# Kernel optimization log

Hardware: AMD Instinct MI355X
Metric: run time of the kernel (lower is better)

Reference implementation:

```python
import jax, jax.numpy as jnp
import numpy as np

T, IO, H, M = 8192, 32, 256, 4  # timesteps, io_width, hidden_width, max ponder steps
EPS = 0.01  # ACT halting epsilon


def setup_inputs() -> dict:
    key = jax.random.key(0)
    ks = jax.random.split(key, 8)
    sc = 0.05
    return {
        "x": jax.random.normal(ks[0], (T, IO), jnp.float32),
        "h0": jnp.zeros((H,), jnp.float32),                       # act1_h initial state
        "Wp": jax.random.normal(ks[1], (H, IO), jnp.float32) * sc,  # input_processing Linear
        "bp": jnp.zeros((H,), jnp.float32),
        "Wx": jax.random.normal(ks[2], (H, H + 1), jnp.float32) * sc,  # ACT cell input weights (+1 first-step flag)
        "Ws": jax.random.normal(ks[3], (H, H), jnp.float32) * sc,      # ACT cell recurrent weights
        "b": jnp.zeros((H,), jnp.float32),
        "wh": jax.random.normal(ks[4], (H,), jnp.float32) * sc,        # halting unit
        "bh": jnp.float32(1.0),
        "Wo": jax.random.normal(ks[5], (IO, H), jnp.float32) * sc,     # ACT output projection
        "bo": jnp.zeros((IO,), jnp.float32),
    }


def reference(x, h0, Wp, bp, Wx, Ws, b, wh, bh, Wo, bo):
    # Faithful translation: per-timestep loop (lax.scan) over the sequence; each step
    # runs input_processing then an ACT (Graves) ponder loop with max M=4 steps.
    # io_noise is identity in eval mode. attention_beam_width=1 => line == current point.
    T_ = x.shape[0]

    def step(carry, x_t):
        h, pc = carry
        lin1 = Wp @ x_t + bp  # [H]
        s = h
        cum = jnp.float32(0.0)
        acc_s = jnp.zeros_like(h)
        acc_y = jnp.zeros_like(bo)
        n_up = jnp.float32(0.0)
        rem = jnp.float32(0.0)
        still = jnp.bool_(True)
        for n in range(M):  # fixed small ponder loop, masked ACT halting
            flag = jnp.full((1,), 1.0 if n == 0 else 0.0, lin1.dtype)
            inp = jnp.concatenate([lin1, flag])  # [H+1]
            s = jnp.tanh(Wx @ inp + Ws @ s + b)
            p = jax.nn.sigmoid(wh @ s + bh)
            halt = (cum + p > 1.0 - EPS) | (n == M - 1)
            w = jnp.where(still, jnp.where(halt, 1.0 - cum, p), 0.0)
            acc_s = acc_s + w * s
            acc_y = acc_y + w * (Wo @ s + bo)
            rem = rem + jnp.where(still & halt, 1.0 - cum, 0.0)
            n_up = n_up + jnp.where(still, 1.0, 0.0)
            cum = cum + w
            still = still & jnp.logical_not(halt)
        ponder = n_up + rem  # N(t) + R(t)
        pc = (pc + ponder) / jnp.float32(T_)  # matches the in-loop division in the original forward
        return (acc_s, pc), acc_y

    (_, pc), ys = jax.lax.scan(step, (h0, jnp.float32(0.0)), x)
    return ys, pc
```

## Files before the change

### kernel.cpp

```cpp
#include <hip/hip_runtime.h>


#define T_  8192
#define IO_ 32
#define H_  256

typedef __attribute__((ext_vector_type(2))) float v2f;

template<int CTRL>
__device__ __forceinline__ float dpp_addf(float x) {
    int xi = __builtin_bit_cast(int, x);
    int d = __builtin_amdgcn_update_dpp(xi, xi, CTRL, 0xF, 0xF, false);
    return x + __builtin_bit_cast(float, d);
}
template<int CTRL>
__device__ __forceinline__ float dpp_get(float x) {
    int xi = __builtin_bit_cast(int, x);
    int d = __builtin_amdgcn_update_dpp(xi, xi, CTRL, 0xF, 0xF, false);
    return __builtin_bit_cast(float, d);
}
__device__ __forceinline__ float swz_xor4(float x) {
    return __builtin_bit_cast(float,
        __builtin_amdgcn_ds_swizzle(__builtin_bit_cast(int, x), 0x101F));
}
__device__ __forceinline__ void bar_lds() {
    asm volatile("s_waitcnt lgkmcnt(0)\n\ts_barrier" ::: "memory");
    __builtin_amdgcn_sched_barrier(0);
}

__device__ __forceinline__ float mv_reduce(const v2f (&wt)[8][8], const v2f (&sc)[8]) {
    float v[8];
    #pragma unroll
    for (int k = 0; k < 8; ++k) {
        v2f a = wt[k][0] * sc[0];
        #pragma unroll
        for (int q = 1; q < 8; ++q) a += wt[k][q] * sc[q];
        v[k] = a.x + a.y;
    }
    v[0] += dpp_get<0x128>(v[4]);
    v[1] += dpp_get<0x128>(v[5]);
    v[2] += dpp_get<0x128>(v[6]);
    v[3] += dpp_get<0x128>(v[7]);
    v[0] += dpp_get<0x4E>(v[2]);
    v[1] += dpp_get<0x4E>(v[3]);
    v[0] += swz_xor4(v[1]);
    v[0] += dpp_get<0xB1>(v[0]);
    return v[0];
}

__global__ void k_prep(const float* __restrict__ Wx,
                       const float* __restrict__ Wp,
                       const float* __restrict__ bp,
                       const float* __restrict__ b,
                       float* __restrict__ WxpT, float* __restrict__ cvec) {
    int h = blockIdx.x;
    int t = threadIdx.x;
    __shared__ float wxrow[H_];
    for (int j = t; j < H_; j += 64) wxrow[j] = Wx[h * (H_ + 1) + j];
    __syncthreads();
    if (t < IO_) {
        float acc = 0.0f;
        for (int j = 0; j < H_; ++j) acc += wxrow[j] * Wp[j * IO_ + t];
        WxpT[t * H_ + h] = acc;
    } else if (t == IO_) {
        float acc = b[h];
        for (int j = 0; j < H_; ++j) acc += wxrow[j] * bp[j];
        cvec[h] = acc;
    }
}

__global__ void k_u(const float* __restrict__ x,
                    const float* __restrict__ WxpT,
                    const float* __restrict__ cvec,
                    float* __restrict__ U) {
    int t0 = blockIdx.x * 8;
    int tid = threadIdx.x;
    __shared__ float xsf[8 * IO_];
    xsf[tid] = x[(size_t)t0 * IO_ + tid];
    __syncthreads();
    int h = tid;
    float base = cvec[h];
    const float L2E2 = 2.8853900817779268f;
    for (int tt = 0; tt < 8; ++tt) {
        float acc = base;
        #pragma unroll
        for (int io = 0; io < IO_; ++io)
            acc += WxpT[io * H_ + h] * xsf[tt * IO_ + io];
        U[(size_t)(t0 + tt) * H_ + h] = acc * L2E2;
    }
}

__global__ __launch_bounds__(512, 2) void act_chain(
    const float* __restrict__ Ws,
    const float* __restrict__ Wx,
    const float* __restrict__ wh,
    const float* __restrict__ bh1,
    const float* __restrict__ h0,
    float* __restrict__ UAcc,
    float* __restrict__ cumArr,
    float* __restrict__ pc_out)
{
    __shared__ __align__(16) float sbuf[2][320];
    __shared__ __align__(16) float plds[2][8];

    const int tid = threadIdx.x;
    const int w   = tid >> 6;
    const int l   = tid & 63;
    const int cb  = l & 15;
    const int g   = ((l & 8) >> 1) | (l & 2) | ((l & 4) >> 2);
    const int rbase = w * 32 + (l >> 4) * 8;
    const int r_own = rbase + g;
    const int swidx = (r_own >> 4) * 20 + (r_own & 15);

    const float L2E  = 1.4426950408889634f;
    const float L2E2 = 2.8853900817779268f;

    v2f wt[8][8];
    #pragma unroll
    for (int k = 0; k < 8; ++k) {
        const float4* s4 = (const float4*)(Ws + (size_t)(rbase + (k ^ g)) * H_ + cb * 16);
        #pragma unroll
        for (int q = 0; q < 4; ++q) {
            float4 f = s4[q];
            wt[k][2 * q]     = (v2f){f.x * L2E2, f.y * L2E2};
            wt[k][2 * q + 1] = (v2f){f.z * L2E2, f.w * L2E2};
        }
    }

    const float wlf = Wx[(size_t)r_own * (H_ + 1) + H_] * L2E2;
    const float whp = wh[r_own] * (-L2E);
    const float bhp = -bh1[0] * L2E;
    const float thresh = 1.0f - 0.01f;

    float zh;
    {
        v2f sc[8];
        const float4* hp = (const float4*)(h0 + cb * 16);
        #pragma unroll
        for (int q = 0; q < 4; ++q) {
            float4 f = hp[q];
            sc[2 * q]     = (v2f){f.x, f.y};
            sc[2 * q + 1] = (v2f){f.z, f.w};
        }
        zh = mv_reduce(wt, sc);
    }

    int wb = 0, pp = 0;
    float pc = 0.0f;
    float un_cur = UAcc[r_own];

    #pragma unroll 1
    for (int t = 0; t < T_; ++t) {
        const int tn = (t + 1 < T_) ? t + 1 : t;
        const float un_nxt = UAcc[(size_t)tn * H_ + r_own];

        float accs = 0.0f, zacc = 0.0f;
        float cum = 0.0f, nup = 0.0f, remt = 0.0f;
        float zin = zh;
        float uadd = un_cur + wlf;

        #pragma unroll 1
        for (int n = 0; n < 4; ++n) {
            float e = __builtin_amdgcn_exp2f(zin + uadd);
            float s = __builtin_fmaf(-2.0f, __builtin_amdgcn_rcpf(e + 1.0f), 1.0f);
            sbuf[wb][swidx] = s;
            float part = whp * s;
            part = dpp_addf<0x4E>(part);
            part = dpp_addf<0x124>(part);
            part = dpp_addf<0x128>(part);
            part = dpp_addf<0x142>(part);
            part = dpp_addf<0x143>(part);
            if (l == 63) plds[pp][w] = part;
            bar_lds();
            const float4* sp = (const float4*)(&sbuf[wb][cb * 20]);
            const float4* pr = (const float4*)(&plds[pp][0]);
            wb ^= 1; pp ^= 1;
            float4 qa = pr[0], qb = pr[1];
            float4 f0 = sp[0], f1 = sp[1], f2 = sp[2], f3 = sp[3];
            v2f sc[8] = {{f0.x, f0.y}, {f0.z, f0.w}, {f1.x, f1.y}, {f1.z, f1.w},
                         {f2.x, f2.y}, {f2.z, f2.w}, {f3.x, f3.y}, {f3.z, f3.w}};
            float z = mv_reduce(wt, sc);
            float dot = ((qa.x + qa.y) + (qa.z + qa.w)) +
                        ((qb.x + qb.y) + (qb.z + qb.w));
            float p = __builtin_amdgcn_rcpf(1.0f + __builtin_amdgcn_exp2f(dot + bhp));
            bool halt = (cum + p > thresh) || (n == 3);
            float hw = 1.0f - cum;
            float wn = halt ? hw : p;
            accs = __builtin_fmaf(wn, s, accs);
            zacc = __builtin_fmaf(wn, z, zacc);
            nup += 1.0f;
            cum += wn;
            if (halt) { remt = hw; break; }
            zin = z;
            uadd = un_cur;
        }

        pc = (pc + nup + remt) * (1.0f / (float)T_);
        zh = zacc;
        if ((l & 1) == 0) UAcc[(size_t)t * H_ + r_own] = accs;
        if (tid == 0) cumArr[t] = cum;
        un_cur = un_nxt;
    }
    if (tid == 0) pc_out[0] = pc;
}

__global__ void k_out(const float* __restrict__ AccS,
                      const float* __restrict__ Wo,
                      const float* __restrict__ bo,
                      const float* __restrict__ cumArr,
                      float* __restrict__ ys) {
    int t0 = blockIdx.x * 8;
    int tid = threadIdx.x;
    __shared__ float wo[IO_ * 257];
    __shared__ float as[8 * 260];
    for (int i = tid; i < IO_ * H_; i += 256) {
        int o = i / H_, h = i % H_;
        wo[o * 257 + h] = Wo[i];
    }
    for (int i = tid; i < 8 * H_; i += 256) {
        int tt = i / H_, h = i % H_;
        as[tt * 260 + h] = AccS[(size_t)t0 * H_ + i];
    }
    __syncthreads();
    int tt = tid >> 5, o = tid & 31;
    float acc = cumArr[t0 + tt] * bo[o];
    #pragma unroll 4
    for (int h = 0; h < H_; ++h) acc += wo[o * 257 + h] * as[tt * 260 + h];
    ys[(size_t)(t0 + tt) * IO_ + o] = acc;
}

extern "C" void kernel_launch(void* const* d_in, const int* in_sizes, int n_in,
                              void* d_out, int out_size, void* d_ws, size_t ws_size,
                              hipStream_t stream) {
    const float* x  = (const float*)d_in[0];
    const float* h0 = (const float*)d_in[1];
    const float* Wp = (const float*)d_in[2];
    const float* bp = (const float*)d_in[3];
    const float* Wx = (const float*)d_in[4];
    const float* Ws = (const float*)d_in[5];
    const float* b  = (const float*)d_in[6];
    const float* wh = (const float*)d_in[7];
    const float* bh = (const float*)d_in[8];
    const float* Wo = (const float*)d_in[9];
    const float* bo = (const float*)d_in[10];
    float* out = (float*)d_out;

    char* ws = (char*)d_ws;
    float* WxpT = (float*)ws;
    float* cvec = (float*)(ws + 32768);
    float* cumA = (float*)(ws + 33792);
    float* UAcc = (float*)(ws + 66560);

    k_prep<<<H_, 64, 0, stream>>>(Wx, Wp, bp, b, WxpT, cvec);
    k_u<<<T_ / 8, 256, 0, stream>>>(x, WxpT, cvec, UAcc);
    act_chain<<<1, 512, 0, stream>>>(Ws, Wx, wh, bh, h0, UAcc, cumA,
                                     out + (size_t)T_ * IO_);
    k_out<<<T_ / 8, 256, 0, stream>>>(UAcc, Wo, bo, cumA, out);
}
```

Measured before the change: 13.16 ms.

## Unroll ACT ponder loop in pairs and rework lane mapping for DPP-only reductions

Replaces the dynamic ponder loop with explicit rounds: two rounds always run, and the last two run only when the step has not halted. Halting logic becomes branch-light. The lane-to-row mapping changes to a rotated layout so the matvec reduction uses only row-level DPP ops instead of a ds_swizzle. This cuts LDS swizzle latency and loop overhead on the serial critical path. In exchange, the second round always runs even when step 0 would halt. Code size also grows.

```diff
diff --git a/kernel.cpp b/kernel.cpp
--- a/kernel.cpp
+++ b/kernel.cpp
@@ -19,10 +19,6 @@
     int d = __builtin_amdgcn_update_dpp(xi, xi, CTRL, 0xF, 0xF, false);
     return __builtin_bit_cast(float, d);
 }
-__device__ __forceinline__ float swz_xor4(float x) {
-    return __builtin_bit_cast(float,
-        __builtin_amdgcn_ds_swizzle(__builtin_bit_cast(int, x), 0x101F));
-}
 __device__ __forceinline__ void bar_lds() {
     asm volatile("s_waitcnt lgkmcnt(0)\n\ts_barrier" ::: "memory");
     __builtin_amdgcn_sched_barrier(0);
@@ -37,14 +33,15 @@
         for (int q = 1; q < 8; ++q) a += wt[k][q] * sc[q];
         v[k] = a.x + a.y;
     }
-    v[0] += dpp_get<0x128>(v[4]);
-    v[1] += dpp_get<0x128>(v[5]);
-    v[2] += dpp_get<0x128>(v[6]);
-    v[3] += dpp_get<0x128>(v[7]);
-    v[0] += dpp_get<0x4E>(v[2]);
-    v[1] += dpp_get<0x4E>(v[3]);
-    v[0] += swz_xor4(v[1]);
-    v[0] += dpp_get<0xB1>(v[0]);
+    #pragma unroll
+    for (int k = 0; k < 8; ++k) v[k] = dpp_addf<0x128>(v[k]);
+    v[0] += dpp_get<0x124>(v[4]);
+    v[1] += dpp_get<0x124>(v[5]);
+    v[2] += dpp_get<0x124>(v[6]);
+    v[3] += dpp_get<0x124>(v[7]);
+    v[0] += dpp_get<0x121>(v[1]);
+    v[0] += dpp_get<0x122>(v[2]);
+    v[0] += dpp_get<0x123>(v[3]);
     return v[0];
 }
 
@@ -106,11 +103,11 @@
     const int tid = threadIdx.x;
     const int w   = tid >> 6;
     const int l   = tid & 63;
-    const int cb  = l & 15;
-    const int g   = ((l & 8) >> 1) | (l & 2) | ((l & 4) >> 2);
-    const int rbase = w * 32 + (l >> 4) * 8;
-    const int r_own = rbase + g;
+    const int m   = l & 15;
+    const int rbase = w * 32 + ((l >> 4) & 3) * 8;
+    const int r_own = rbase + (m & 7);
     const int swidx = (r_own >> 4) * 20 + (r_own & 15);
+    const bool pub  = (l & 8) == 0;
 
     const float L2E  = 1.4426950408889634f;
     const float L2E2 = 2.8853900817779268f;
@@ -118,7 +115,8 @@
     v2f wt[8][8];
     #pragma unroll
     for (int k = 0; k < 8; ++k) {
-        const float4* s4 = (const float4*)(Ws + (size_t)(rbase + (k ^ g)) * H_ + cb * 16);
+        const int rk = rbase + ((k + m) & 7);
+        const float4* s4 = (const float4*)(Ws + (size_t)rk * H_ + m * 16);
         #pragma unroll
         for (int q = 0; q < 4; ++q) {
             float4 f = s4[q];
@@ -130,12 +128,12 @@
     const float wlf = Wx[(size_t)r_own * (H_ + 1) + H_] * L2E2;
     const float whp = wh[r_own] * (-L2E);
     const float bhp = -bh1[0] * L2E;
-    const float thresh = 1.0f - 0.01f;
+    const float thresh = 0.99f;
 
     float zh;
     {
         v2f sc[8];
-        const float4* hp = (const float4*)(h0 + cb * 16);
+        const float4* hp = (const float4*)(h0 + m * 16);
         #pragma unroll
         for (int q = 0; q < 4; ++q) {
             float4 f = hp[q];
@@ -145,61 +143,81 @@
         zh = mv_reduce(wt, sc);
     }
 
-    int wb = 0, pp = 0;
     float pc = 0.0f;
     float un_cur = UAcc[r_own];
+    float u0_cur = un_cur + wlf;
+
+    auto round = [&](int WB, int PP, float in, float& z, float& p) -> float {
+        float e = __builtin_amdgcn_exp2f(in);
+        float s = __builtin_fmaf(-2.0f, __builtin_amdgcn_rcpf(e + 1.0f), 1.0f);
+        if (pub) sbuf[WB][swidx] = s;
+        float part = whp * s;
+        part = dpp_addf<0x121>(part);
+        part = dpp_addf<0x122>(part);
+        part = dpp_addf<0x124>(part);
+        part = dpp_addf<0x142>(part);
+        part = dpp_addf<0x143>(part);
+        if (l == 63) plds[PP][w] = part;
+        bar_lds();
+        const float4* sp = (const float4*)(&sbuf[WB][m * 20]);
+        float4 f0 = sp[0], f1 = sp[1], f2 = sp[2], f3 = sp[3];
+        const float4* pr = (const float4*)(&plds[PP][0]);
+        float4 qa = pr[0], qb = pr[1];
+        v2f sc[8] = {{f0.x, f0.y}, {f0.z, f0.w}, {f1.x, f1.y}, {f1.z, f1.w},
+                     {f2.x, f2.y}, {f2.z, f2.w}, {f3.x, f3.y}, {f3.z, f3.w}};
+        z = mv_reduce(wt, sc);
+        float dot = ((qa.x + qa.y) + (qa.z + qa.w)) +
+                    ((qb.x + qb.y) + (qb.z + qb.w));
+        p = __builtin_amdgcn_rcpf(1.0f + __builtin_amdgcn_exp2f(dot + bhp));
+        return s;
+    };
 
     #pragma unroll 1
     for (int t = 0; t < T_; ++t) {
         const int tn = (t + 1 < T_) ? t + 1 : t;
         const float un_nxt = UAcc[(size_t)tn * H_ + r_own];
 
-        float accs = 0.0f, zacc = 0.0f;
-        float cum = 0.0f, nup = 0.0f, remt = 0.0f;
-        float zin = zh;
-        float uadd = un_cur + wlf;
-
-        #pragma unroll 1
-        for (int n = 0; n < 4; ++n) {
-            float e = __builtin_amdgcn_exp2f(zin + uadd);
-            float s = __builtin_fmaf(-2.0f, __builtin_amdgcn_rcpf(e + 1.0f), 1.0f);
-            sbuf[wb][swidx] = s;
-            float part = whp * s;
-            part = dpp_addf<0x4E>(part);
-            part = dpp_addf<0x124>(part);
-            part = dpp_addf<0x128>(part);
-            part = dpp_addf<0x142>(part);
-            part = dpp_addf<0x143>(part);
-            if (l == 63) plds[pp][w] = part;
-            bar_lds();
-            const float4* sp = (const float4*)(&sbuf[wb][cb * 20]);
-            const float4* pr = (const float4*)(&plds[pp][0]);
-            wb ^= 1; pp ^= 1;
-            float4 qa = pr[0], qb = pr[1];
-            float4 f0 = sp[0], f1 = sp[1], f2 = sp[2], f3 = sp[3];
-            v2f sc[8] = {{f0.x, f0.y}, {f0.z, f0.w}, {f1.x, f1.y}, {f1.z, f1.w},
-                         {f2.x, f2.y}, {f2.z, f2.w}, {f3.x, f3.y}, {f3.z, f3.w}};
-            float z = mv_reduce(wt, sc);
-            float dot = ((qa.x + qa.y) + (qa.z + qa.w)) +
-                        ((qb.x + qb.y) + (qb.z + qb.w));
-            float p = __builtin_amdgcn_rcpf(1.0f + __builtin_amdgcn_exp2f(dot + bhp));
-            bool halt = (cum + p > thresh) || (n == 3);
-            float hw = 1.0f - cum;
-            float wn = halt ? hw : p;
-            accs = __builtin_fmaf(wn, s, accs);
-            zacc = __builtin_fmaf(wn, z, zacc);
-            nup += 1.0f;
-            cum += wn;
-            if (halt) { remt = hw; break; }
-            zin = z;
-            uadd = un_cur;
+        float z0, p0, z1, p1;
+        float s0 = round(0, 0, zh + u0_cur, z0, p0);
+        float s1 = round(1, 1, z0 + un_cur, z1, p1);
+
+        bool  halt0  = p0 > thresh;
+        float w0     = halt0 ? 1.0f : p0;
+        bool  still1 = !halt0;
+        float cum1   = w0;
+        bool  halt1  = (cum1 + p1 > thresh);
+        float w1     = still1 ? (halt1 ? 1.0f - cum1 : p1) : 0.0f;
+        float accs   = __builtin_fmaf(w1, s1, w0 * s0);
+        float zacc   = __builtin_fmaf(w1, z1, w0 * z0);
+        float cum    = cum1 + w1;
+        float nup    = still1 ? 2.0f : 1.0f;
+        float rem    = halt0 ? 1.0f : (halt1 ? 1.0f - cum1 : 0.0f);
+
+        if (still1 && !halt1) {
+            float z2, p2, z3, p3;
+            float s2 = round(0, 0, z1 + un_cur, z2, p2);
+            bool  halt2 = (cum + p2 > thresh);
+            float w2    = halt2 ? 1.0f - cum : p2;
+            float rem2  = halt2 ? 1.0f - cum : 0.0f;
+            accs = __builtin_fmaf(w2, s2, accs);
+            zacc = __builtin_fmaf(w2, z2, zacc);
+            float cum3  = cum + w2;
+            bool  still3 = !halt2;
+            float s3 = round(1, 1, z2 + un_cur, z3, p3);
+            float w3 = still3 ? (1.0f - cum3) : 0.0f;
+            accs = __builtin_fmaf(w3, s3, accs);
+            zacc = __builtin_fmaf(w3, z3, zacc);
+            rem  = rem2 + w3;
+            cum  = cum3 + w3;
+            nup  = still3 ? 4.0f : 3.0f;
         }
 
-        pc = (pc + nup + remt) * (1.0f / (float)T_);
+        pc = (pc + nup + rem) * (1.0f / (float)T_);
         zh = zacc;
-        if ((l & 1) == 0) UAcc[(size_t)t * H_ + r_own] = accs;
+        if (pub) UAcc[(size_t)t * H_ + r_own] = accs;
         if (tid == 0) cumArr[t] = cum;
         un_cur = un_nxt;
+        u0_cur = un_nxt + wlf;
     }
     if (tid == 0) pc_out[0] = pc;
 }
```

New measurement: 12.87 ms. -2.2%, faster.
